# Optimization experiments

Hardware: AMD Instinct MI355X
Metric: run time of the kernel (lower is better)

The kernel has to match this reference:

```python
import jax, jax.numpy as jnp
import numpy as np

B, S, D = 2, 2048, 2048
H, G = 32, 8           # num_heads, num_groups
HD = D // H            # head_dim = 64
GS = H // G            # group_size = 4


def setup_inputs() -> dict:
    key = jax.random.key(0)
    ks = jax.random.split(key, 11)
    s = 0.02
    return {
        "x": jax.random.normal(ks[0], (B, S, D), dtype=jnp.float32),
        "kv": jax.random.normal(ks[1], (B, S, D), dtype=jnp.float32),
        "Wq": jax.random.normal(ks[2], (D, D), dtype=jnp.float32) * s,
        "bq": jnp.zeros((D,), dtype=jnp.float32),
        "Wk": jax.random.normal(ks[3], (D, G * HD), dtype=jnp.float32) * s,
        "bk": jnp.zeros((G * HD,), dtype=jnp.float32),
        "Wv": jax.random.normal(ks[4], (D, G * HD), dtype=jnp.float32) * s,
        "bv": jnp.zeros((G * HD,), dtype=jnp.float32),
        "Wo": jax.random.normal(ks[5], (D, D), dtype=jnp.float32) * s,
        "bo": jnp.zeros((D,), dtype=jnp.float32),
        "expanding_context": 0,
    }


def reference(x, kv, Wq, bq, Wk, bk, Wv, bv, Wo, bo, expanding_context):
    # expanding_context is ignored when use_kv_cache=False (matches torch module)
    b, s, d = x.shape
    q = (x @ Wq + bq).reshape(b, s, H, HD).transpose(0, 2, 1, 3)      # [B,H,S,HD]
    k = (kv @ Wk + bk).reshape(b, s, G, HD).transpose(0, 2, 1, 3)     # [B,G,S,HD]
    v = (kv @ Wv + bv).reshape(b, s, G, HD).transpose(0, 2, 1, 3)     # [B,G,S,HD]
    # repeat_interleave KV heads to match query heads
    k = jnp.repeat(k, GS, axis=1)                                      # [B,H,S,HD]
    v = jnp.repeat(v, GS, axis=1)
    scale = 1.0 / jnp.sqrt(jnp.array(HD, dtype=x.dtype))
    scores = jnp.einsum("bhqd,bhkd->bhqk", q, k) * scale              # [B,H,S,S]
    causal = jnp.tril(jnp.ones((s, s), dtype=bool))                    # True where allowed
    scores = jnp.where(causal[None, None], scores, jnp.finfo(x.dtype).min)
    attn = jax.nn.softmax(scores, axis=-1)
    out = jnp.einsum("bhqk,bhkd->bhqd", attn, v)                      # [B,H,S,HD]
    out = out.transpose(0, 2, 1, 3).reshape(b, s, D)                  # [B,S,D]
    return out @ Wo + bo
```

## Files before the change

kernel.cpp:

```cpp
#include <hip/hip_runtime.h>
#include <hip/hip_bf16.h>
#include <stdint.h>

namespace {
constexpr int CB = 2, CS = 2048, CD = 2048, CH = 32, CG = 8, CHD = 64, CGS = 4;

typedef __bf16 bf16x8 __attribute__((ext_vector_type(8)));
typedef float f32x4 __attribute__((ext_vector_type(4)));
typedef float f32x16 __attribute__((ext_vector_type(16)));
typedef uint32_t u32x4 __attribute__((ext_vector_type(4)));

__device__ inline uint16_t f2bf(float f) {
  uint32_t u = __float_as_uint(f);
  u += 0x7fffu + ((u >> 16) & 1u);
  return (uint16_t)(u >> 16);
}

__device__ inline void gload_lds16(const void* g, void* l) {
  __builtin_amdgcn_global_load_lds(
      (const __attribute__((address_space(1))) void*)g,
      (__attribute__((address_space(3))) void*)l, 16, 0, 0);
}

__device__ inline uint32_t cvtpk_bf16(float lo, float hi) {
  uint32_t r;
  asm("v_cvt_pk_bf16_f32 %0, %1, %2" : "=v"(r) : "v"(lo), "v"(hi));
  return r;
}
__device__ inline void pl32swap(uint32_t& a, uint32_t& b) {
  asm("v_permlane32_swap_b32 %0, %1" : "+v"(a), "+v"(b));
}
}

__global__ __launch_bounds__(256) void cast_both_kernel(
    const float* __restrict__ x, const float* __restrict__ kv,
    uint16_t* __restrict__ xb, uint16_t* __restrict__ kvb, int nel) {
  int i = (blockIdx.x * 256 + threadIdx.x) * 4;
  const float* in;
  uint16_t* out;
  if (i < nel) { in = x + i; out = xb + i; }
  else         { in = kv + (i - nel); out = kvb + (i - nel); }
  const float4 v = *(const float4*)in;
  ushort4 o;
  o.x = f2bf(v.x); o.y = f2bf(v.y); o.z = f2bf(v.z); o.w = f2bf(v.w);
  *(ushort4*)out = o;
}

__global__ __launch_bounds__(256) void transpose_all_kernel(
    const float* __restrict__ Wq, const float* __restrict__ Wk,
    const float* __restrict__ Wv, const float* __restrict__ Wo,
    uint16_t* __restrict__ out) {
  __shared__ uint16_t tile[32][33];
  const int gn0 = blockIdx.x * 32;
  const int k0 = blockIdx.y * 32;
  const float* in;
  int Nr, start;
  if (gn0 < 2048)      { in = Wq; Nr = 2048; start = 0; }
  else if (gn0 < 2560) { in = Wk; Nr = 512;  start = 2048; }
  else if (gn0 < 3072) { in = Wv; Nr = 512;  start = 2560; }
  else                 { in = Wo; Nr = 2048; start = 3072; }
  const int n0 = gn0 - start;
  const int tx = threadIdx.x & 31, tg = threadIdx.x >> 5;
#pragma unroll
  for (int rr = 0; rr < 4; ++rr) {
    int k = tg * 4 + rr;
    tile[k][tx] = f2bf(in[(size_t)(k0 + k) * Nr + n0 + tx]);
  }
  __syncthreads();
#pragma unroll
  for (int rr = 0; rr < 4; ++rr) {
    int n = tg * 4 + rr;
    out[(size_t)(gn0 + n) * CD + k0 + tx] = tile[tx][n];
  }
}

__global__ __launch_bounds__(256, 2) void gemm_qkv_kernel(
    const uint16_t* __restrict__ xb, const uint16_t* __restrict__ kvb,
    const uint16_t* __restrict__ WT,
    const float* __restrict__ bq, const float* __restrict__ bk,
    const float* __restrict__ bv,
    uint16_t* __restrict__ Qb, uint16_t* __restrict__ Kb,
    uint16_t* __restrict__ VTb) {
  constexpr int BM = 128, BN = 128, BK = 32, K = 2048, NT = K / BK;
  constexpr int ASZ = BM * BK;
  constexpr int BSZ = BN * BK;
  constexpr int BUFSZ = ASZ + BSZ;
  __shared__ uint16_t smem[3 * BUFSZ];
  const int tid = threadIdx.x;
  const int w = tid >> 6, l = tid & 63;
  const int wr = w >> 1, wc = w & 1;
  const int l15 = l & 15, lq = l >> 4;

  const int gx = gridDim.x;
  int bid = blockIdx.y * gx + blockIdx.x;
  const int nwg = gx * gridDim.y;
  bid = (bid & 7) * (nwg >> 3) + (bid >> 3);
  const int m0 = (bid / gx) * BM, n0 = (bid % gx) * BN;
  const uint16_t* A = (n0 < 2048) ? xb : kvb;

  auto stage = [&](int buf, int kt) {
    uint16_t* base = smem + buf * BUFSZ;
    const int k0 = kt * BK;
#pragma unroll
    for (int i = 0; i < 2; ++i) {
      int g = i * 256 + tid;
      int row = g >> 2, slot = g & 3;
      int kq = slot ^ ((row >> 1) & 3);
      gload_lds16(A + (size_t)(m0 + row) * K + k0 + kq * 8, base + g * 8);
    }
#pragma unroll
    for (int i = 0; i < 2; ++i) {
      int g = i * 256 + tid;
      int row = g >> 2, slot = g & 3;
      int kq = slot ^ ((row >> 1) & 3);
      gload_lds16(WT + (size_t)(n0 + row) * K + k0 + kq * 8,
                  base + ASZ + g * 8);
    }
  };

  int aOff[4], bOff[4];
#pragma unroll
  for (int m = 0; m < 4; ++m) {
    int row = wr * 64 + m * 16 + l15;
    aOff[m] = (row * BK + (lq ^ ((row >> 1) & 3)) * 8) * 2;
  }
#pragma unroll
  for (int n = 0; n < 4; ++n) {
    int row = wc * 64 + n * 16 + l15;
    bOff[n] = ASZ * 2 + (row * BK + (lq ^ ((row >> 1) & 3)) * 8) * 2;
  }

  f32x4 acc[4][4] = {};

  stage(0, 0);
  stage(1, 1);

  int bt = 0, bs = 2;
  for (int t = 0; t < NT; ++t) {
    if (t < NT - 1) asm volatile("s_waitcnt vmcnt(4)" ::: "memory");
    else            asm volatile("s_waitcnt vmcnt(0)" ::: "memory");
    __builtin_amdgcn_s_barrier();
    asm volatile("" ::: "memory");

    const char* buf = (const char*)(smem + bt * BUFSZ);
    bf16x8 af[4], bfr[4];
#pragma unroll
    for (int m = 0; m < 4; ++m) af[m] = *(const bf16x8*)(buf + aOff[m]);
#pragma unroll
    for (int n = 0; n < 4; ++n) bfr[n] = *(const bf16x8*)(buf + bOff[n]);

    if (t + 2 < NT) stage(bs, t + 2);

    __builtin_amdgcn_s_setprio(1);
#pragma unroll
    for (int m = 0; m < 4; ++m)
#pragma unroll
      for (int n = 0; n < 4; ++n)
        acc[m][n] = __builtin_amdgcn_mfma_f32_16x16x32_bf16(
            af[m], bfr[n], acc[m][n], 0, 0, 0);
    __builtin_amdgcn_s_setprio(0);

    bt = bt == 2 ? 0 : bt + 1;
    bs = bs == 2 ? 0 : bs + 1;
  }

#pragma unroll
  for (int m = 0; m < 4; ++m)
#pragma unroll
    for (int n = 0; n < 4; ++n)
#pragma unroll
      for (int r = 0; r < 4; ++r) {
        int gm = m0 + wr * 64 + m * 16 + lq * 4 + r;
        int gn = n0 + wc * 64 + n * 16 + l15;
        int b = gm >> 11, s = gm & (CS - 1);
        if (n0 < 2048) {
          float v = (acc[m][n][r] + bq[gn]) * (0.125f * 1.44269504088896340736f);
          int h = gn >> 6, hd = gn & 63;
          Qb[(((size_t)(b * CH + h)) * CS + s) * CHD + hd] = f2bf(v);
        } else if (n0 < 2560) {
          int gn2 = gn - 2048;
          float v = acc[m][n][r] + bk[gn2];
          int gh = gn2 >> 6, hd = gn2 & 63;
          Kb[(((size_t)(b * CG + gh)) * CS + s) * CHD + hd] = f2bf(v);
        } else {
          int gn2 = gn - 2560;
          float v = acc[m][n][r] + bv[gn2];
          int gh = gn2 >> 6, hd = gn2 & 63;
          VTb[(((size_t)(b * CG + gh)) * CHD + hd) * CS + s] = f2bf(v);
        }
      }
}

__global__ __launch_bounds__(256, 2) void gemm_out_kernel(
    const uint16_t* __restrict__ A, const uint16_t* __restrict__ Bt,
    const float* __restrict__ bias, float* __restrict__ Cout,
    int M, int N, int Kdim) {
  constexpr int BM = 128, BN = 128, BK = 32, K = 2048, NT = K / BK;
  constexpr int ASZ = BM * BK;
  constexpr int BSZ = BN * BK;
  constexpr int BUFSZ = ASZ + BSZ;
  __shared__ uint16_t smem[3 * BUFSZ];
  const int tid = threadIdx.x;
  const int w = tid >> 6, l = tid & 63;
  const int wr = w >> 1, wc = w & 1;
  const int l15 = l & 15, lq = l >> 4;

  const int gx = gridDim.x;
  int bid = blockIdx.y * gx + blockIdx.x;
  const int nwg = gx * gridDim.y;
  bid = (bid & 7) * (nwg >> 3) + (bid >> 3);
  const int m0 = (bid / gx) * BM, n0 = (bid % gx) * BN;

  auto stage = [&](int buf, int kt) {
    uint16_t* base = smem + buf * BUFSZ;
    const int k0 = kt * BK;
#pragma unroll
    for (int i = 0; i < 2; ++i) {
      int g = i * 256 + tid;
      int row = g >> 2, slot = g & 3;
      int kq = slot ^ ((row >> 1) & 3);
      gload_lds16(A + (size_t)(m0 + row) * K + k0 + kq * 8, base + g * 8);
    }
#pragma unroll
    for (int i = 0; i < 2; ++i) {
      int g = i * 256 + tid;
      int row = g >> 2, slot = g & 3;
      int kq = slot ^ ((row >> 1) & 3);
      gload_lds16(Bt + (size_t)(n0 + row) * K + k0 + kq * 8,
                  base + ASZ + g * 8);
    }
  };

  int aOff[4], bOff[4];
#pragma unroll
  for (int m = 0; m < 4; ++m) {
    int row = wr * 64 + m * 16 + l15;
    aOff[m] = (row * BK + (lq ^ ((row >> 1) & 3)) * 8) * 2;
  }
#pragma unroll
  for (int n = 0; n < 4; ++n) {
    int row = wc * 64 + n * 16 + l15;
    bOff[n] = ASZ * 2 + (row * BK + (lq ^ ((row >> 1) & 3)) * 8) * 2;
  }

  f32x4 acc[4][4] = {};

  stage(0, 0);
  stage(1, 1);

  int bt = 0, bs = 2;
  for (int t = 0; t < NT; ++t) {
    if (t < NT - 1) asm volatile("s_waitcnt vmcnt(4)" ::: "memory");
    else            asm volatile("s_waitcnt vmcnt(0)" ::: "memory");
    __builtin_amdgcn_s_barrier();
    asm volatile("" ::: "memory");

    const char* buf = (const char*)(smem + bt * BUFSZ);
    bf16x8 af[4], bfr[4];
#pragma unroll
    for (int m = 0; m < 4; ++m) af[m] = *(const bf16x8*)(buf + aOff[m]);
#pragma unroll
    for (int n = 0; n < 4; ++n) bfr[n] = *(const bf16x8*)(buf + bOff[n]);

    if (t + 2 < NT) stage(bs, t + 2);

    __builtin_amdgcn_s_setprio(1);
#pragma unroll
    for (int m = 0; m < 4; ++m)
#pragma unroll
      for (int n = 0; n < 4; ++n)
        acc[m][n] = __builtin_amdgcn_mfma_f32_16x16x32_bf16(
            af[m], bfr[n], acc[m][n], 0, 0, 0);
    __builtin_amdgcn_s_setprio(0);

    bt = bt == 2 ? 0 : bt + 1;
    bs = bs == 2 ? 0 : bs + 1;
  }

#pragma unroll
  for (int m = 0; m < 4; ++m)
#pragma unroll
    for (int n = 0; n < 4; ++n)
#pragma unroll
      for (int r = 0; r < 4; ++r) {
        int gm = m0 + wr * 64 + m * 16 + lq * 4 + r;
        int gn = n0 + wc * 64 + n * 16 + l15;
        Cout[(size_t)gm * N + gn] = acc[m][n][r] + bias[gn];
      }
}

__global__ __launch_bounds__(256) void flash_attn_kernel(
    const uint16_t* __restrict__ Q, const uint16_t* __restrict__ K,
    const uint16_t* __restrict__ VT, uint16_t* __restrict__ Aout) {
  constexpr int NQB = CS / 128;
  __shared__ __align__(16) uint16_t Ksm[2][64 * 64];
  __shared__ __align__(16) uint16_t Vsm[2][64 * 64];
  const int tid = threadIdx.x, w = tid >> 6, l = tid & 63;
  const int l31 = l & 31, hi = l >> 5;
  const int x = blockIdx.x;
  const int h = blockIdx.y, b = blockIdx.z, g = h >> 2;

  const uint16_t* Qbase = Q + ((size_t)(b * CH + h)) * CS * CHD;
  const uint16_t* Kbase = K + ((size_t)(b * CG + g)) * CS * CHD;
  const uint16_t* Vbase = VT + ((size_t)(b * CG + g)) * CHD * CS;

  const int srow = tid >> 3, sslot = tid & 7;
  const int skq = sslot ^ (srow & 7);
  const uint16_t* kSrc0 = Kbase + (size_t)srow * CHD + skq * 8;
  const uint16_t* kSrc1 = kSrc0 + 32 * CHD;
  const uint16_t* vSrc0 = Vbase + (size_t)srow * CS + skq * 8;
  const uint16_t* vSrc1 = vSrc0 + 32 * CS;
  uint16_t* kDst0 = &Ksm[0][0] + tid * 8;
  uint16_t* vDst0 = &Vsm[0][0] + tid * 8;

  int qkOff[2][4];
#pragma unroll
  for (int c = 0; c < 2; ++c)
#pragma unroll
    for (int kc = 0; kc < 4; ++kc) {
      int row = c * 32 + l31;
      qkOff[c][kc] = ((row * 64 + kc * 16 + hi * 8) * 2) ^ ((row & 7) << 4);
    }

  auto stage = [&](int buf, int kt) {
    const size_t ko = (size_t)kt * 64 * CHD;
    const int vo = kt * 64;
    uint16_t* kd = kDst0 + buf * 64 * 64;
    uint16_t* vd = vDst0 + buf * 64 * 64;
    gload_lds16(kSrc0 + ko, kd);
    gload_lds16(kSrc1 + ko, kd + 2048);
    gload_lds16(vSrc0 + vo, vd);
    gload_lds16(vSrc1 + vo, vd + 2048);
  };

#pragma unroll 1
  for (int job = 0; job < 2; ++job) {
    const int qb = job == 0 ? (NQB - 1 - x) : x;
    const int qrow = qb * 128 + w * 32 + l31;
    const int wtop = qb * 128 + w * 32 + 31;

    bf16x8 qf[4];
#pragma unroll
    for (int kc = 0; kc < 4; ++kc)
      qf[kc] = *(const bf16x8*)(Qbase + (size_t)qrow * CHD + kc * 16 + hi * 8);

    f32x16 o0 = {}, o1 = {};
    float mrun = -3e38f, lrun = 0.f;
    const int nt = 2 * qb + 2;

    stage(0, 0);
    asm volatile("s_waitcnt vmcnt(0)" ::: "memory");
    __syncthreads();

    for (int kt = 0; kt < nt; ++kt) {
      const int cur = kt & 1;
      if (kt + 1 < nt) stage(cur ^ 1, kt + 1);

      if (kt * 64 <= wtop) {
        const char* ksmb = (const char*)Ksm[cur];
        const char* vsmb = (const char*)Vsm[cur];

        f32x16 p0 = {}, p1 = {};
        __builtin_amdgcn_s_setprio(1);
#pragma unroll
        for (int kc = 0; kc < 4; ++kc) {
          bf16x8 ka0 = *(const bf16x8*)(ksmb + qkOff[0][kc]);
          bf16x8 ka1 = *(const bf16x8*)(ksmb + qkOff[1][kc]);
          p0 = __builtin_amdgcn_mfma_f32_32x32x16_bf16(ka0, qf[kc], p0, 0, 0, 0);
          p1 = __builtin_amdgcn_mfma_f32_32x32x16_bf16(ka1, qf[kc], p1, 0, 0, 0);
        }
        __builtin_amdgcn_s_setprio(0);

        const bool need_mask = (kt * 64 + 63 > qb * 128 + w * 32);
        float pmax = -3e38f;
        if (need_mask) {
#pragma unroll
          for (int r = 0; r < 16; ++r) {
            int keyb = kt * 64 + (r & 3) + 8 * (r >> 2) + 4 * hi;
            if (keyb > qrow) p0[r] = -3e38f;
            if (keyb + 32 > qrow) p1[r] = -3e38f;
          }
        }
#pragma unroll
        for (int r = 0; r < 16; ++r) {
          pmax = fmaxf(pmax, p0[r]);
          pmax = fmaxf(pmax, p1[r]);
        }
        pmax = fmaxf(pmax, __shfl_xor(pmax, 32));

        if (!__all(pmax <= mrun + 8.f)) {
          float mnew = fmaxf(mrun, pmax);
          float alpha = __builtin_amdgcn_exp2f(mrun - mnew);
#pragma unroll
          for (int r = 0; r < 16; ++r) { o0[r] *= alpha; o1[r] *= alpha; }
          lrun *= alpha;
          mrun = mnew;
        }
        float s = 0.f;
#pragma unroll
        for (int r = 0; r < 16; ++r) {
          float e0 = __builtin_amdgcn_exp2f(p0[r] - mrun);
          float e1 = __builtin_amdgcn_exp2f(p1[r] - mrun);
          p0[r] = e0; p1[r] = e1;
          s += e0 + e1;
        }
        s += __shfl_xor(s, 32);
        lrun += s;

        u32x4 paw[4];
#pragma unroll
        for (int k = 0; k < 4; ++k) {
          const int base = (k & 1) * 8;
          const f32x16& pc = (k >> 1) ? p1 : p0;
          uint32_t c01 = cvtpk_bf16(pc[base + 0], pc[base + 1]);
          uint32_t c23 = cvtpk_bf16(pc[base + 2], pc[base + 3]);
          uint32_t c45 = cvtpk_bf16(pc[base + 4], pc[base + 5]);
          uint32_t c67 = cvtpk_bf16(pc[base + 6], pc[base + 7]);
          pl32swap(c01, c45);
          pl32swap(c23, c67);
          paw[k] = (u32x4){c01, c23, c45, c67};
        }

        __builtin_amdgcn_s_setprio(1);
#pragma unroll
        for (int ks = 0; ks < 4; ++ks) {
          bf16x8 vb0 = *(const bf16x8*)(vsmb + qkOff[0][ks]);
          bf16x8 vb1 = *(const bf16x8*)(vsmb + qkOff[1][ks]);
          bf16x8 pb = __builtin_bit_cast(bf16x8, paw[ks]);
          o0 = __builtin_amdgcn_mfma_f32_32x32x16_bf16(vb0, pb, o0, 0, 0, 0);
          o1 = __builtin_amdgcn_mfma_f32_32x32x16_bf16(vb1, pb, o1, 0, 0, 0);
        }
        __builtin_amdgcn_s_setprio(0);
      }

      asm volatile("s_waitcnt vmcnt(0)" ::: "memory");
      __syncthreads();
    }

    float invl = 1.f / lrun;
    uint16_t* orow = Aout + ((size_t)b * CS + qrow) * CD + (size_t)h * CHD;
#pragma unroll
    for (int k = 0; k < 8; ++k) {
      int reg = 2 * k;
      int hd = (reg & 3) + 8 * (reg >> 2) + 4 * hi;
      *(uint32_t*)(orow + hd) = cvtpk_bf16(o0[reg] * invl, o0[reg + 1] * invl);
      *(uint32_t*)(orow + hd + 32) = cvtpk_bf16(o1[reg] * invl, o1[reg + 1] * invl);
    }
  }
}

extern "C" void kernel_launch(void* const* d_in, const int* in_sizes, int n_in,
                              void* d_out, int out_size, void* d_ws, size_t ws_size,
                              hipStream_t stream) {
  const float* x = (const float*)d_in[0];
  const float* kv = (const float*)d_in[1];
  const float* Wq = (const float*)d_in[2];
  const float* bq = (const float*)d_in[3];
  const float* Wk = (const float*)d_in[4];
  const float* bk = (const float*)d_in[5];
  const float* Wv = (const float*)d_in[6];
  const float* bv = (const float*)d_in[7];
  const float* Wo = (const float*)d_in[8];
  const float* bo = (const float*)d_in[9];
  float* out = (float*)d_out;

  char* ws = (char*)d_ws;
  uint16_t* xb = (uint16_t*)ws;   ws += (size_t)CB * CS * CD * 2;
  uint16_t* kvb = (uint16_t*)ws;  ws += (size_t)CB * CS * CD * 2;
  uint16_t* WqT = (uint16_t*)ws;  ws += (size_t)CD * CD * 2;
  uint16_t* WkT = (uint16_t*)ws;  ws += (size_t)(CG * CHD) * CD * 2;
  uint16_t* WvT = (uint16_t*)ws;  ws += (size_t)(CG * CHD) * CD * 2;
  uint16_t* WoT = (uint16_t*)ws;  ws += (size_t)CD * CD * 2;
  uint16_t* Qb = (uint16_t*)ws;   ws += (size_t)CB * CH * CS * CHD * 2;
  uint16_t* Kb = (uint16_t*)ws;   ws += (size_t)CB * CG * CS * CHD * 2;
  uint16_t* VTb = (uint16_t*)ws;  ws += (size_t)CB * CG * CHD * CS * 2;
  uint16_t* attnb = (uint16_t*)ws;
  (void)WkT; (void)WvT;

  const int NTOK = CB * CS;
  const int nel = CB * CS * CD;

  cast_both_kernel<<<2 * nel / 4 / 256, 256, 0, stream>>>(x, kv, xb, kvb, nel);
  transpose_all_kernel<<<dim3(5120 / 32, CD / 32), 256, 0, stream>>>(
      Wq, Wk, Wv, Wo, WqT);

  gemm_qkv_kernel<<<dim3(3072 / 128, NTOK / 128), 256, 0, stream>>>(
      xb, kvb, WqT, bq, bk, bv, Qb, Kb, VTb);

  flash_attn_kernel<<<dim3(CS / 256, CH, CB), 256, 0, stream>>>(Qb, Kb, VTb, attnb);

  gemm_out_kernel<<<dim3(CD / 128, NTOK / 128), 256, 0, stream>>>(
      attnb, WoT, bo, out, NTOK, CD, CD);
}
```

Baseline: 209.3 us.

## Enlarge flash attention KV tile to 128 keys and set two blocks per CU

The flash-attention KV tile grows from 64 to 128 keys, so each iteration computes four 32-key score blocks and eight PV MFMA steps. The K/V shared-memory staging and the swizzled offsets are rewritten to match (the V swizzle now uses a 16-slot XOR). This halves the number of loop iterations, barriers and softmax rescale passes. In exchange it raises register pressure, and it drops the per-wave skip of fully masked tiles, so the diagonal tiles do more wasted work. Launch bounds now request two blocks per CU.

```diff
diff --git a/kernel.cpp b/kernel.cpp
--- a/kernel.cpp
+++ b/kernel.cpp
@@ -289,12 +289,13 @@
       }
 }
 
-__global__ __launch_bounds__(256) void flash_attn_kernel(
+__global__ __launch_bounds__(256, 2) void flash_attn_kernel(
     const uint16_t* __restrict__ Q, const uint16_t* __restrict__ K,
     const uint16_t* __restrict__ VT, uint16_t* __restrict__ Aout) {
   constexpr int NQB = CS / 128;
-  __shared__ __align__(16) uint16_t Ksm[2][64 * 64];
-  __shared__ __align__(16) uint16_t Vsm[2][64 * 64];
+  constexpr int KV = 128;
+  __shared__ __align__(16) uint16_t Ksm[2][KV * CHD];
+  __shared__ __align__(16) uint16_t Vsm[2][CHD * KV];
   const int tid = threadIdx.x, w = tid >> 6, l = tid & 63;
   const int l31 = l & 31, hi = l >> 5;
   const int x = blockIdx.x;
@@ -304,40 +305,47 @@
   const uint16_t* Kbase = K + ((size_t)(b * CG + g)) * CS * CHD;
   const uint16_t* Vbase = VT + ((size_t)(b * CG + g)) * CHD * CS;
 
-  const int srow = tid >> 3, sslot = tid & 7;
-  const int skq = sslot ^ (srow & 7);
-  const uint16_t* kSrc0 = Kbase + (size_t)srow * CHD + skq * 8;
-  const uint16_t* kSrc1 = kSrc0 + 32 * CHD;
-  const uint16_t* vSrc0 = Vbase + (size_t)srow * CS + skq * 8;
-  const uint16_t* vSrc1 = vSrc0 + 32 * CS;
-  uint16_t* kDst0 = &Ksm[0][0] + tid * 8;
-  uint16_t* vDst0 = &Vsm[0][0] + tid * 8;
-
-  int qkOff[2][4];
-#pragma unroll
-  for (int c = 0; c < 2; ++c)
+  auto stage = [&](int buf, int kt) {
+#pragma unroll
+    for (int i = 0; i < 4; ++i) {
+      int gK = i * 256 + tid;
+      int rowK = gK >> 3, slotK = gK & 7;
+      int kqK = slotK ^ (rowK & 7);
+      gload_lds16(Kbase + ((size_t)kt * KV + rowK) * CHD + kqK * 8,
+                  &Ksm[buf][gK * 8]);
+    }
+#pragma unroll
+    for (int i = 0; i < 4; ++i) {
+      int gV = i * 256 + tid;
+      int rowV = gV >> 4, slotV = gV & 15;
+      int kqV = slotV ^ (rowV & 15);
+      gload_lds16(Vbase + (size_t)rowV * CS + kt * KV + kqV * 8,
+                  &Vsm[buf][gV * 8]);
+    }
+  };
+
+  int kOff[4][4];
+#pragma unroll
+  for (int c = 0; c < 4; ++c)
 #pragma unroll
     for (int kc = 0; kc < 4; ++kc) {
       int row = c * 32 + l31;
-      qkOff[c][kc] = ((row * 64 + kc * 16 + hi * 8) * 2) ^ ((row & 7) << 4);
-    }
-
-  auto stage = [&](int buf, int kt) {
-    const size_t ko = (size_t)kt * 64 * CHD;
-    const int vo = kt * 64;
-    uint16_t* kd = kDst0 + buf * 64 * 64;
-    uint16_t* vd = vDst0 + buf * 64 * 64;
-    gload_lds16(kSrc0 + ko, kd);
-    gload_lds16(kSrc1 + ko, kd + 2048);
-    gload_lds16(vSrc0 + vo, vd);
-    gload_lds16(vSrc1 + vo, vd + 2048);
-  };
+      kOff[c][kc] = ((row * CHD + kc * 16 + hi * 8) * 2) ^ ((row & 7) << 4);
+    }
+  int vOff[2][8];
+#pragma unroll
+  for (int c = 0; c < 2; ++c)
+#pragma unroll
+    for (int ks = 0; ks < 8; ++ks) {
+      int row = c * 32 + l31;
+      vOff[c][ks] = ((row * KV + ks * 16 + hi * 8) * 2) ^ ((row & 15) << 4);
+    }
 
 #pragma unroll 1
   for (int job = 0; job < 2; ++job) {
     const int qb = job == 0 ? (NQB - 1 - x) : x;
     const int qrow = qb * 128 + w * 32 + l31;
-    const int wtop = qb * 128 + w * 32 + 31;
+    const int wbase = qb * 128 + w * 32;
 
     bf16x8 qf[4];
 #pragma unroll
@@ -346,7 +354,7 @@
 
     f32x16 o0 = {}, o1 = {};
     float mrun = -3e38f, lrun = 0.f;
-    const int nt = 2 * qb + 2;
+    const int nt = qb + 1;
 
     stage(0, 0);
     asm volatile("s_waitcnt vmcnt(0)" ::: "memory");
@@ -356,82 +364,88 @@
       const int cur = kt & 1;
       if (kt + 1 < nt) stage(cur ^ 1, kt + 1);
 
-      if (kt * 64 <= wtop) {
-        const char* ksmb = (const char*)Ksm[cur];
-        const char* vsmb = (const char*)Vsm[cur];
-
-        f32x16 p0 = {}, p1 = {};
-        __builtin_amdgcn_s_setprio(1);
-#pragma unroll
-        for (int kc = 0; kc < 4; ++kc) {
-          bf16x8 ka0 = *(const bf16x8*)(ksmb + qkOff[0][kc]);
-          bf16x8 ka1 = *(const bf16x8*)(ksmb + qkOff[1][kc]);
-          p0 = __builtin_amdgcn_mfma_f32_32x32x16_bf16(ka0, qf[kc], p0, 0, 0, 0);
-          p1 = __builtin_amdgcn_mfma_f32_32x32x16_bf16(ka1, qf[kc], p1, 0, 0, 0);
+      const char* ksmb = (const char*)Ksm[cur];
+      const char* vsmb = (const char*)Vsm[cur];
+
+      f32x16 p0 = {}, p1 = {}, p2 = {}, p3 = {};
+      __builtin_amdgcn_s_setprio(1);
+#pragma unroll
+      for (int kc = 0; kc < 4; ++kc) {
+        bf16x8 ka0 = *(const bf16x8*)(ksmb + kOff[0][kc]);
+        bf16x8 ka1 = *(const bf16x8*)(ksmb + kOff[1][kc]);
+        bf16x8 ka2 = *(const bf16x8*)(ksmb + kOff[2][kc]);
+        bf16x8 ka3 = *(const bf16x8*)(ksmb + kOff[3][kc]);
+        p0 = __builtin_amdgcn_mfma_f32_32x32x16_bf16(ka0, qf[kc], p0, 0, 0, 0);
+        p1 = __builtin_amdgcn_mfma_f32_32x32x16_bf16(ka1, qf[kc], p1, 0, 0, 0);
+        p2 = __builtin_amdgcn_mfma_f32_32x32x16_bf16(ka2, qf[kc], p2, 0, 0, 0);
+        p3 = __builtin_amdgcn_mfma_f32_32x32x16_bf16(ka3, qf[kc], p3, 0, 0, 0);
+      }
+      __builtin_amdgcn_s_setprio(0);
+
+      const bool need_mask = (kt * KV + KV - 1 > wbase);
+      if (need_mask) {
+#pragma unroll
+        for (int r = 0; r < 16; ++r) {
+          int keyb = kt * KV + (r & 3) + 8 * (r >> 2) + 4 * hi;
+          if (keyb > qrow) p0[r] = -3e38f;
+          if (keyb + 32 > qrow) p1[r] = -3e38f;
+          if (keyb + 64 > qrow) p2[r] = -3e38f;
+          if (keyb + 96 > qrow) p3[r] = -3e38f;
         }
-        __builtin_amdgcn_s_setprio(0);
-
-        const bool need_mask = (kt * 64 + 63 > qb * 128 + w * 32);
-        float pmax = -3e38f;
-        if (need_mask) {
-#pragma unroll
-          for (int r = 0; r < 16; ++r) {
-            int keyb = kt * 64 + (r & 3) + 8 * (r >> 2) + 4 * hi;
-            if (keyb > qrow) p0[r] = -3e38f;
-            if (keyb + 32 > qrow) p1[r] = -3e38f;
-          }
-        }
-#pragma unroll
-        for (int r = 0; r < 16; ++r) {
-          pmax = fmaxf(pmax, p0[r]);
-          pmax = fmaxf(pmax, p1[r]);
-        }
-        pmax = fmaxf(pmax, __shfl_xor(pmax, 32));
-
-        if (!__all(pmax <= mrun + 8.f)) {
-          float mnew = fmaxf(mrun, pmax);
-          float alpha = __builtin_amdgcn_exp2f(mrun - mnew);
-#pragma unroll
-          for (int r = 0; r < 16; ++r) { o0[r] *= alpha; o1[r] *= alpha; }
-          lrun *= alpha;
-          mrun = mnew;
-        }
-        float s = 0.f;
-#pragma unroll
-        for (int r = 0; r < 16; ++r) {
-          float e0 = __builtin_amdgcn_exp2f(p0[r] - mrun);
-          float e1 = __builtin_amdgcn_exp2f(p1[r] - mrun);
-          p0[r] = e0; p1[r] = e1;
-          s += e0 + e1;
-        }
-        s += __shfl_xor(s, 32);
-        lrun += s;
-
-        u32x4 paw[4];
-#pragma unroll
-        for (int k = 0; k < 4; ++k) {
-          const int base = (k & 1) * 8;
-          const f32x16& pc = (k >> 1) ? p1 : p0;
-          uint32_t c01 = cvtpk_bf16(pc[base + 0], pc[base + 1]);
-          uint32_t c23 = cvtpk_bf16(pc[base + 2], pc[base + 3]);
-          uint32_t c45 = cvtpk_bf16(pc[base + 4], pc[base + 5]);
-          uint32_t c67 = cvtpk_bf16(pc[base + 6], pc[base + 7]);
-          pl32swap(c01, c45);
-          pl32swap(c23, c67);
-          paw[k] = (u32x4){c01, c23, c45, c67};
-        }
-
-        __builtin_amdgcn_s_setprio(1);
-#pragma unroll
-        for (int ks = 0; ks < 4; ++ks) {
-          bf16x8 vb0 = *(const bf16x8*)(vsmb + qkOff[0][ks]);
-          bf16x8 vb1 = *(const bf16x8*)(vsmb + qkOff[1][ks]);
-          bf16x8 pb = __builtin_bit_cast(bf16x8, paw[ks]);
-          o0 = __builtin_amdgcn_mfma_f32_32x32x16_bf16(vb0, pb, o0, 0, 0, 0);
-          o1 = __builtin_amdgcn_mfma_f32_32x32x16_bf16(vb1, pb, o1, 0, 0, 0);
-        }
-        __builtin_amdgcn_s_setprio(0);
-      }
+      }
+      float pmax = -3e38f;
+#pragma unroll
+      for (int r = 0; r < 16; ++r) {
+        pmax = fmaxf(pmax, fmaxf(fmaxf(p0[r], p1[r]), fmaxf(p2[r], p3[r])));
+      }
+      pmax = fmaxf(pmax, __shfl_xor(pmax, 32));
+
+      if (!__all(pmax <= mrun + 8.f)) {
+        float mnew = fmaxf(mrun, pmax);
+        float alpha = __builtin_amdgcn_exp2f(mrun - mnew);
+#pragma unroll
+        for (int r = 0; r < 16; ++r) { o0[r] *= alpha; o1[r] *= alpha; }
+        lrun *= alpha;
+        mrun = mnew;
+      }
+      float s = 0.f;
+#pragma unroll
+      for (int r = 0; r < 16; ++r) {
+        float e0 = __builtin_amdgcn_exp2f(p0[r] - mrun);
+        float e1 = __builtin_amdgcn_exp2f(p1[r] - mrun);
+        float e2 = __builtin_amdgcn_exp2f(p2[r] - mrun);
+        float e3 = __builtin_amdgcn_exp2f(p3[r] - mrun);
+        p0[r] = e0; p1[r] = e1; p2[r] = e2; p3[r] = e3;
+        s += (e0 + e1) + (e2 + e3);
+      }
+      s += __shfl_xor(s, 32);
+      lrun += s;
+
+      u32x4 paw[8];
+#pragma unroll
+      for (int k = 0; k < 8; ++k) {
+        const int base = (k & 1) * 8;
+        const int c = k >> 1;
+        const f32x16& pc = (c == 0) ? p0 : (c == 1) ? p1 : (c == 2) ? p2 : p3;
+        uint32_t c01 = cvtpk_bf16(pc[base + 0], pc[base + 1]);
+        uint32_t c23 = cvtpk_bf16(pc[base + 2], pc[base + 3]);
+        uint32_t c45 = cvtpk_bf16(pc[base + 4], pc[base + 5]);
+        uint32_t c67 = cvtpk_bf16(pc[base + 6], pc[base + 7]);
+        pl32swap(c01, c45);
+        pl32swap(c23, c67);
+        paw[k] = (u32x4){c01, c23, c45, c67};
+      }
+
+      __builtin_amdgcn_s_setprio(1);
+#pragma unroll
+      for (int ks = 0; ks < 8; ++ks) {
+        bf16x8 vb0 = *(const bf16x8*)(vsmb + vOff[0][ks]);
+        bf16x8 vb1 = *(const bf16x8*)(vsmb + vOff[1][ks]);
+        bf16x8 pb = __builtin_bit_cast(bf16x8, paw[ks]);
+        o0 = __builtin_amdgcn_mfma_f32_32x32x16_bf16(vb0, pb, o0, 0, 0, 0);
+        o1 = __builtin_amdgcn_mfma_f32_32x32x16_bf16(vb1, pb, o1, 0, 0, 0);
+      }
+      __builtin_amdgcn_s_setprio(0);
 
       asm volatile("s_waitcnt vmcnt(0)" ::: "memory");
       __syncthreads();
```

Measured after the change: 200.7 us. -4.1%, faster.
